# Performance work log

Measured on AMD Instinct MI355X. Metric: run time of the kernel, lower is better.

## Reference

```python
import jax, jax.numpy as jnp
import numpy as np

B, L = 4, 2048
D_MODEL, D_INNER, D_STATE, DT_RANK, D_CONV = 1024, 2048, 16, 64, 4


def setup_inputs() -> dict:
    key = jax.random.key(0)
    ks = jax.random.split(key, 10)
    s = lambda k, shape, sc: jax.random.normal(k, shape, dtype=jnp.float32) * sc
    return {
        "x": s(ks[0], (B, L, D_MODEL), 1.0),
        "W_in": s(ks[1], (2 * D_INNER, D_MODEL), D_MODEL ** -0.5),
        "conv_w": s(ks[2], (D_INNER, D_CONV), D_CONV ** -0.5),
        "conv_b": s(ks[3], (D_INNER,), 0.02),
        "A_log": jnp.log(jnp.arange(1, D_STATE + 1, dtype=jnp.float32)),
        "D": jnp.ones((D_INNER,), dtype=jnp.float32),
        "W_x": s(ks[4], (DT_RANK + 2 * D_STATE, D_INNER), D_INNER ** -0.5),
        "W_dt": s(ks[5], (D_INNER, DT_RANK), DT_RANK ** -0.5),
        "b_dt": s(ks[6], (D_INNER,), 0.02) - 4.0,  # softplus -> small positive dt
        "W_out": s(ks[7], (D_MODEL, D_INNER), D_INNER ** -0.5),
    }


def reference(x, W_in, conv_w, conv_b, A_log, D, W_x, W_dt, b_dt, W_out):
    Bb, Ll, _ = x.shape
    # input projection, split into ssm branch and gate branch
    xz = x @ W_in.T                       # (B, L, 2*Di)
    xr, z = jnp.split(xz, 2, axis=-1)     # (B, L, Di) each
    # depthwise causal conv1d (torch pads both sides then slices [:L])
    xc = jax.lax.conv_general_dilated(
        xr.transpose(0, 2, 1),            # (B, Di, L)
        conv_w[:, None, :],               # (Di, 1, K)
        window_strides=(1,),
        padding=[(D_CONV - 1, 0)],
        dimension_numbers=("NCH", "OIH", "NCH"),
        feature_group_count=D_INNER,
    ) + conv_b[None, :, None]
    xs = jax.nn.silu(xc.transpose(0, 2, 1))  # (B, L, Di)
    # input-dependent dt, B, C
    x_dbl = xs @ W_x.T                        # (B, L, dt_rank + 2*S)
    dt_r, b_sel, c_sel = jnp.split(x_dbl, [DT_RANK, DT_RANK + D_STATE], axis=-1)
    dt = jax.nn.softplus(dt_r @ W_dt.T + b_dt)  # (B, L, Di)
    a_diag = -jnp.exp(A_log)                    # (S,)

    def step(h, inp):
        dt_t, b_t, c_t, x_t = inp                       # (B,Di),(B,S),(B,S),(B,Di)
        a_bar = jnp.exp(dt_t[:, :, None] * a_diag)      # (B, Di, S)
        h = a_bar * h + (dt_t * x_t)[:, :, None] * b_t[:, None, :]
        y = jnp.einsum("bds,bs->bd", h, c_t) + D * x_t
        return h, y

    h0 = jnp.zeros((Bb, D_INNER, D_STATE), dtype=x.dtype)
    _, ys = jax.lax.scan(
        step, h0,
        (dt.transpose(1, 0, 2), b_sel.transpose(1, 0, 2),
         c_sel.transpose(1, 0, 2), xs.transpose(1, 0, 2)),
    )
    y = ys.transpose(1, 0, 2)                           # (B, L, Di)
    return (y * jax.nn.silu(z)) @ W_out.T               # (B, L, d_model)
```

## Files before the change

kernel.cpp:

```cpp
#include <hip/hip_runtime.h>
#include <math.h>

typedef unsigned short u16;
typedef unsigned int u32;

constexpr int Bb = 4, Ll = 2048, DM = 1024, DI = 2048, DS = 16, DTR = 64, KC = 4;
constexpr int M = Bb * Ll;
constexpr int NPAD = 128;
constexpr int NCHUNK = 16;
constexpr int LC = Ll / NCHUNK;
constexpr int LDXZ = 4096;

__device__ __forceinline__ float b2f(u16 u) {
    return __uint_as_float(((u32)u) << 16);
}
__device__ __forceinline__ u16 f2b(float f) {
    u32 x = __float_as_uint(f);
    u32 r = (x + 0x7fffu + ((x >> 16) & 1u)) >> 16;
    return (u16)r;
}

typedef __attribute__((ext_vector_type(8))) short short8;
typedef __attribute__((ext_vector_type(4))) short short4v;
typedef __attribute__((ext_vector_type(4))) float floatx4;

__device__ __forceinline__ void gload16(const u16* g, u16* l) {
    __builtin_amdgcn_global_load_lds(
        (const __attribute__((address_space(1))) void*)g,
        (__attribute__((address_space(3))) void*)l,
        16, 0, 0);
}

__device__ __forceinline__ void pow_tree(float a, float* aa) {
    float a2 = a * a, a4 = a2 * a2, a8 = a4 * a4;
    aa[0] = a;        aa[1] = a2;       aa[2] = a * a2;   aa[3] = a4;
    aa[4] = a * a4;   aa[5] = a2 * a4;  aa[6] = aa[2] * a4; aa[7] = a8;
    aa[8] = a * a8;   aa[9] = a2 * a8;  aa[10] = aa[2] * a8; aa[11] = a4 * a8;
    aa[12] = aa[4] * a8; aa[13] = aa[5] * a8; aa[14] = aa[6] * a8; aa[15] = a8 * a8;
}

template<int OUTM>
__global__ __launch_bounds__(512, 2) void gemm256(
    const u16* __restrict__ A, const u16* __restrict__ Bm,
    void* __restrict__ Cv,
    int K, int lda, int ldb, int ldc)
{
    __shared__ alignas(16) u16 ldsA[4][256 * 32];
    __shared__ alignas(16) u16 ldsB[4][256 * 32];

    const int lane = threadIdx.x & 63;
    const int wave = threadIdx.x >> 6;
    const int wr = wave >> 2;
    const int wc = wave & 3;
    const int m0 = blockIdx.y * 256;
    const int n0 = blockIdx.x * 256;

    const int lrow = lane >> 2;
    const int skc  = (((lane & 3) + (lane >> 3)) & 3) * 8;
    const u16* pA = A  + (size_t)(m0 + wave * 32 + lrow) * lda + skc;
    const u16* pB = Bm + (size_t)(n0 + wave * 32 + lrow) * ldb + skc;
    const int ldst = wave * 1024;

    const int r16 = lane & 15;
    const int quad = lane >> 4;
    const int slot = (quad + 4 - ((r16 >> 1) & 3)) & 3;
    const int aoff = (wr * 128 + r16) * 32 + slot * 8;
    const int boff = (wc * 64  + r16) * 32 + slot * 8;

    const int NT = K >> 5;

    floatx4 acc[8][4] = {};

#pragma unroll
    for (int t = 0; t < 3; ++t) {
        gload16(pA + t * 32,            &ldsA[t][ldst]);
        gload16(pA + t * 32 + 16 * lda, &ldsA[t][ldst + 512]);
        gload16(pB + t * 32,            &ldsB[t][ldst]);
        gload16(pB + t * 32 + 16 * ldb, &ldsB[t][ldst + 512]);
    }
    asm volatile("s_waitcnt vmcnt(8)" ::: "memory");
    __builtin_amdgcn_sched_barrier(0);
    __builtin_amdgcn_s_barrier();

    for (int t = 0; t < NT; ++t) {
        const u16* la = &ldsA[t & 3][aoff];
        const u16* lb = &ldsB[t & 3][boff];
        short8 af[8], bf[4];

#pragma unroll
        for (int i = 0; i < 4; ++i) af[i] = *(const short8*)(la + i * 512);
#pragma unroll
        for (int j = 0; j < 4; ++j) bf[j] = *(const short8*)(lb + j * 512);
        if (t + 3 < NT) {
            const u16* s = pA + (t + 3) * 32;
            u16* d = &ldsA[(t + 3) & 3][ldst];
            gload16(s, d);
            gload16(s + 16 * lda, d + 512);
        }
        __builtin_amdgcn_sched_barrier(0);
        __builtin_amdgcn_s_barrier();
        asm volatile("s_waitcnt lgkmcnt(0)" ::: "memory");
        __builtin_amdgcn_sched_barrier(0);
        __builtin_amdgcn_s_setprio(1);
#pragma unroll
        for (int i = 0; i < 4; ++i)
#pragma unroll
            for (int j = 0; j < 4; ++j)
                acc[i][j] = __builtin_amdgcn_mfma_f32_16x16x32_bf16(
                    af[i], bf[j], acc[i][j], 0, 0, 0);
        __builtin_amdgcn_s_setprio(0);
        __builtin_amdgcn_sched_barrier(0);
        __builtin_amdgcn_s_barrier();

#pragma unroll
        for (int i = 4; i < 8; ++i) af[i] = *(const short8*)(la + i * 512);
        if (t + 3 < NT) {
            const u16* s = pB + (t + 3) * 32;
            u16* d = &ldsB[(t + 3) & 3][ldst];
            gload16(s, d);
            gload16(s + 16 * ldb, d + 512);
        }
        __builtin_amdgcn_sched_barrier(0);
        __builtin_amdgcn_s_barrier();
        asm volatile("s_waitcnt lgkmcnt(0)" ::: "memory");
        __builtin_amdgcn_sched_barrier(0);
        __builtin_amdgcn_s_setprio(1);
#pragma unroll
        for (int i = 4; i < 8; ++i)
#pragma unroll
            for (int j = 0; j < 4; ++j)
                acc[i][j] = __builtin_amdgcn_mfma_f32_16x16x32_bf16(
                    af[i], bf[j], acc[i][j], 0, 0, 0);
        __builtin_amdgcn_s_setprio(0);
        if (t + 3 < NT)      asm volatile("s_waitcnt vmcnt(8)" ::: "memory");
        else if (t + 2 < NT) asm volatile("s_waitcnt vmcnt(4)" ::: "memory");
        else if (t + 1 < NT) asm volatile("s_waitcnt vmcnt(0)" ::: "memory");
        __builtin_amdgcn_sched_barrier(0);
        __builtin_amdgcn_s_barrier();
    }

    const int mw = m0 + wr * 128;
    const int nw = n0 + wc * 64;
    const int rb = quad * 4;
#pragma unroll
    for (int i = 0; i < 8; ++i) {
#pragma unroll
        for (int j = 0; j < 4; ++j) {
            const int n = nw + j * 16 + r16;
#pragma unroll
            for (int r = 0; r < 4; ++r) {
                const int m = mw + i * 16 + rb + r;
                float v = acc[i][j][r];
                if (OUTM == 1)
                    ((float*)Cv)[(size_t)m * ldc + n] = v;
                else
                    ((u16*)Cv)[(size_t)m * ldc + n] = f2b(v);
            }
        }
    }
}

template<int OUTM>
__global__ __launch_bounds__(512, 2) void gemm256n128(
    const u16* __restrict__ A, const u16* __restrict__ Bm,
    void* __restrict__ Cv,
    int K, int lda, int ldb, int ldc)
{
    __shared__ alignas(16) u16 ldsA[4][256 * 32];
    __shared__ alignas(16) u16 ldsB[4][128 * 32];

    const int lane = threadIdx.x & 63;
    const int wave = threadIdx.x >> 6;
    const int wr = wave >> 1;
    const int wc = wave & 1;
    const int m0 = blockIdx.y * 256;
    const int n0 = blockIdx.x * 128;

    const int lrow = lane >> 2;
    const int skc  = (((lane & 3) + (lane >> 3)) & 3) * 8;
    const u16* pA = A  + (size_t)(m0 + wave * 32 + lrow) * lda + skc;
    const u16* pB = Bm + (size_t)(n0 + wave * 16 + lrow) * ldb + skc;
    const int ldstA = wave * 1024;
    const int ldstB = wave * 512;

    const int r16 = lane & 15;
    const int quad = lane >> 4;
    const int slot = (quad + 4 - ((r16 >> 1) & 3)) & 3;
    const int aoff = (wr * 64 + r16) * 32 + slot * 8;
    const int boff = (wc * 64 + r16) * 32 + slot * 8;

    const int NT = K >> 5;

    floatx4 acc[4][4] = {};

#pragma unroll
    for (int t = 0; t < 3; ++t) {
        gload16(pA + t * 32,            &ldsA[t][ldstA]);
        gload16(pA + t * 32 + 16 * lda, &ldsA[t][ldstA + 512]);
        gload16(pB + t * 32,            &ldsB[t][ldstB]);
    }
    asm volatile("s_waitcnt vmcnt(6)" ::: "memory");
    __builtin_amdgcn_sched_barrier(0);
    __builtin_amdgcn_s_barrier();

    for (int t = 0; t < NT; ++t) {
        const u16* la = &ldsA[t & 3][aoff];
        const u16* lb = &ldsB[t & 3][boff];
        short8 af[4], bf[4];
#pragma unroll
        for (int i = 0; i < 4; ++i) af[i] = *(const short8*)(la + i * 512);
#pragma unroll
        for (int j = 0; j < 4; ++j) bf[j] = *(const short8*)(lb + j * 512);
        if (t + 3 < NT) {
            const u16* sa = pA + (t + 3) * 32;
            u16* da = &ldsA[(t + 3) & 3][ldstA];
            gload16(sa, da);
            gload16(sa + 16 * lda, da + 512);
            gload16(pB + (t + 3) * 32, &ldsB[(t + 3) & 3][ldstB]);
        }
        __builtin_amdgcn_sched_barrier(0);
        __builtin_amdgcn_s_barrier();
        asm volatile("s_waitcnt lgkmcnt(0)" ::: "memory");
        __builtin_amdgcn_sched_barrier(0);
        __builtin_amdgcn_s_setprio(1);
#pragma unroll
        for (int i = 0; i < 4; ++i)
#pragma unroll
            for (int j = 0; j < 4; ++j)
                acc[i][j] = __builtin_amdgcn_mfma_f32_16x16x32_bf16(
                    af[i], bf[j], acc[i][j], 0, 0, 0);
        __builtin_amdgcn_s_setprio(0);
        if (t + 3 < NT)      asm volatile("s_waitcnt vmcnt(6)" ::: "memory");
        else if (t + 2 < NT) asm volatile("s_waitcnt vmcnt(3)" ::: "memory");
        else if (t + 1 < NT) asm volatile("s_waitcnt vmcnt(0)" ::: "memory");
        __builtin_amdgcn_sched_barrier(0);
        __builtin_amdgcn_s_barrier();
    }

    const int mw = m0 + wr * 64;
    const int nw = n0 + wc * 64;
    const int rb = quad * 4;
#pragma unroll
    for (int i = 0; i < 4; ++i) {
#pragma unroll
        for (int j = 0; j < 4; ++j) {
            const int n = nw + j * 16 + r16;
#pragma unroll
            for (int r = 0; r < 4; ++r) {
                const int m = mw + i * 16 + rb + r;
                float v = acc[i][j][r];
                if (OUTM == 1)
                    ((float*)Cv)[(size_t)m * ldc + n] = v;
                else
                    ((u16*)Cv)[(size_t)m * ldc + n] = f2b(v);
            }
        }
    }
}

template<int OUTM>
__global__ __launch_bounds__(256) void gemm_bt(
    const u16* __restrict__ A, const u16* __restrict__ Bm,
    void* __restrict__ Cv, const float* __restrict__ bias,
    int K, int lda, int ldb, int ldc)
{
    __shared__ alignas(16) u16 ldsA[128 * 32];
    __shared__ alignas(16) u16 ldsB[128 * 32];

    const int lane = threadIdx.x & 63;
    const int wave = threadIdx.x >> 6;
    const int wr = wave >> 1, wc = wave & 1;
    const int m0 = blockIdx.y * 128;
    const int n0 = blockIdx.x * 128;
    const int koff = (OUTM == 4) ? blockIdx.z * K : 0;

    const int srow = wave * 32 + (lane >> 2);
    const int skc  = (((lane & 3) + (lane >> 3)) & 3) * 8;
    const u16* Ag = A + (size_t)(m0 + srow) * lda + skc + koff;
    const u16* Bg = Bm + (size_t)(n0 + srow) * ldb + skc + koff;
    u16* lA = &ldsA[wave * 1024];
    u16* lB = &ldsB[wave * 1024];

    const int r16 = lane & 15;
    const int quad = lane >> 4;
    const int slot = (quad + 4 - ((r16 >> 1) & 3)) & 3;
    const u16* arow = &ldsA[(wr * 64 + r16) * 32 + slot * 8];
    const u16* brow = &ldsB[(wc * 64 + r16) * 32 + slot * 8];

    floatx4 acc[4][4] = {};

    for (int k0 = 0; k0 < K; k0 += 32) {
        gload16(Ag + k0,                    lA);
        gload16(Ag + k0 + (size_t)16 * lda, lA + 512);
        gload16(Bg + k0,                    lB);
        gload16(Bg + k0 + (size_t)16 * ldb, lB + 512);
        __syncthreads();

        short8 af[4], bf[4];
#pragma unroll
        for (int i = 0; i < 4; i++) af[i] = *(const short8*)(arow + i * 16 * 32);
#pragma unroll
        for (int j = 0; j < 4; j++) bf[j] = *(const short8*)(brow + j * 16 * 32);
#pragma unroll
        for (int i = 0; i < 4; i++)
#pragma unroll
            for (int j = 0; j < 4; j++)
                acc[i][j] = __builtin_amdgcn_mfma_f32_16x16x32_bf16(
                    af[i], bf[j], acc[i][j], 0, 0, 0);
        __syncthreads();
    }

    const int mw = m0 + wr * 64;
    const int nw = n0 + wc * 64;
    const int rb = quad * 4;
#pragma unroll
    for (int i = 0; i < 4; i++) {
#pragma unroll
        for (int j = 0; j < 4; j++) {
            const int n = nw + j * 16 + r16;
#pragma unroll
            for (int r = 0; r < 4; r++) {
                const int m = mw + i * 16 + rb + r;
                float v = acc[i][j][r];
                if (OUTM == 2) {
                    v += bias[n];
                    v = (v > 20.f) ? v : log1pf(__expf(v));
                }
                if (OUTM == 4)
                    ((float*)Cv)[((size_t)blockIdx.z * M + m) * ldc + n] = v;
                else if (OUTM == 1)
                    ((float*)Cv)[(size_t)m * ldc + n] = v;
                else
                    ((u16*)Cv)[(size_t)m * ldc + n] = f2b(v);
            }
        }
    }
}

__global__ __launch_bounds__(256) void redk_gemm3(
    const float* __restrict__ part, u16* __restrict__ xdbl,
    float* __restrict__ bcf)
{
    const int t = blockIdx.x * 256 + threadIdx.x;
    const int n4 = (t & 31) * 4;
    const int m = t >> 5;
    const size_t stride = (size_t)M * NPAD;
    const float* p = part + (size_t)m * NPAD + n4;
    floatx4 acc = *(const floatx4*)(p)
                + *(const floatx4*)(p + stride)
                + *(const floatx4*)(p + 2 * stride)
                + *(const floatx4*)(p + 3 * stride);
    short4v ob;
#pragma unroll
    for (int j = 0; j < 4; j++) ob[j] = (short)f2b(acc[j]);
    *(short4v*)(xdbl + (size_t)m * NPAD + n4) = ob;
    if (n4 >= 64 && n4 < 96)
        *(floatx4*)(bcf + (size_t)m * 32 + (n4 - 64)) = acc;
}

__global__ __launch_bounds__(256) void cvt_f2b(
    const float* __restrict__ in, u16* __restrict__ out, int n)
{
    int i = blockIdx.x * blockDim.x + threadIdx.x;
    if (i < n) out[i] = f2b(in[i]);
}

__global__ __launch_bounds__(256) void prep_weights(
    const float* __restrict__ W_in, const float* __restrict__ W_x,
    const float* __restrict__ W_dt, const float* __restrict__ W_out,
    u16* __restrict__ wibf, u16* __restrict__ wxp,
    u16* __restrict__ wdtb, u16* __restrict__ woutb)
{
    constexpr int N1 = 2 * DI * DM;
    constexpr int N2 = NPAD * DI;
    constexpr int N3 = DI * DTR;
    int idx = blockIdx.x * blockDim.x + threadIdx.x;
    if (idx < N1) {
        wibf[idx] = f2b(W_in[idx]);
    } else if (idx < N1 + N2) {
        int i = idx - N1;
        int r = i >> 11, c = i & 2047;
        wxp[i] = (r < 96) ? f2b(W_x[r * 2048 + c]) : (u16)0;
    } else if (idx < N1 + N2 + N3) {
        int i = idx - N1 - N2;
        wdtb[i] = f2b(W_dt[i]);
    } else {
        int i = idx - N1 - N2 - N3;
        woutb[i] = f2b(W_out[i]);
    }
}

__global__ __launch_bounds__(256) void conv_silu(
    const u16* __restrict__ xz, const float* __restrict__ conv_w,
    const float* __restrict__ conv_b, u16* __restrict__ xs)
{
    const int m = blockIdx.x;
    const int d0 = threadIdx.x * 8;
    const int l = m & (Ll - 1);

    float acc[8];
    {
        floatx4 cb0 = *(const floatx4*)(conv_b + d0);
        floatx4 cb1 = *(const floatx4*)(conv_b + d0 + 4);
#pragma unroll
        for (int j = 0; j < 4; j++) { acc[j] = cb0[j]; acc[4 + j] = cb1[j]; }
    }
    float w[8][KC];
#pragma unroll
    for (int jd = 0; jd < 8; jd++) {
        floatx4 wv = *(const floatx4*)(conv_w + (d0 + jd) * KC);
#pragma unroll
        for (int k = 0; k < KC; k++) w[jd][k] = wv[k];
    }
#pragma unroll
    for (int k = 0; k < KC; k++) {
        int li = l - (KC - 1) + k;
        if (li >= 0) {
            short8 xv = *(const short8*)(xz + (size_t)(m - (KC - 1) + k) * LDXZ + d0);
#pragma unroll
            for (int jd = 0; jd < 8; jd++)
                acc[jd] += b2f((u16)xv[jd]) * w[jd][k];
        }
    }
    short8 o;
#pragma unroll
    for (int jd = 0; jd < 8; jd++) {
        float s = acc[jd] / (1.f + __expf(-acc[jd]));
        o[jd] = (short)f2b(s);
    }
    *(short8*)(xs + (size_t)m * DI + d0) = o;
}

__global__ __launch_bounds__(256) void scan_p1(
    const u16* __restrict__ xzdt, const u16* __restrict__ xs,
    const float* __restrict__ bcf, const float* __restrict__ A_log,
    float* __restrict__ scr_P, float* __restrict__ scr_hend)
{
    __shared__ alignas(16) float bcs[LC * 32];

    const int d = blockIdx.x * 256 + threadIdx.x;
    const int b = blockIdx.y;
    const int c = blockIdx.z;
    const int m0 = b * Ll + c * LC;

    {
        const float* bc_g = bcf + (size_t)m0 * 32;
#pragma unroll
        for (int j = 0; j < 4; j++) {
            int idx = j * 1024 + threadIdx.x * 4;
            *(floatx4*)(bcs + idx) = *(const floatx4*)(bc_g + idx);
        }
    }

    const float ad0 = -__expf(A_log[0]);
    float adl[DS];
    bool fast = true;
#pragma unroll
    for (int s = 0; s < DS; s++) {
        float av = -__expf(A_log[s]);
        adl[s] = av;
        float kr = (float)(s + 1);
        if (fabsf(av / ad0 - kr) > 1e-4f * kr) fast = false;
    }

    const u16* dt_p = xzdt + (size_t)m0 * LDXZ + d;
    const u16* xs_p = xs + (size_t)m0 * DI + d;

    float h[DS] = {};
    float P[DS];
#pragma unroll
    for (int s = 0; s < DS; s++) P[s] = 1.f;
    float sdt = 0.f;

    __syncthreads();

    u16 dt_c = dt_p[0],     xs_c = xs_p[0];
    u16 dt_1 = dt_p[LDXZ],  xs_1 = xs_p[DI];

    if (fast) {
        for (int l = 0; l < LC; l++) {
            u16 dt_2 = dt_p[2 * LDXZ];
            u16 xs_2 = xs_p[2 * DI];
            const float* bl = bcs + l * 32;
            floatx4 B0 = *(const floatx4*)(bl);
            floatx4 B1 = *(const floatx4*)(bl + 4);
            floatx4 B2 = *(const floatx4*)(bl + 8);
            floatx4 B3 = *(const floatx4*)(bl + 12);

            float dtv = b2f(dt_c);
            float xv  = b2f(xs_c);
            float bx = dtv * xv;
            sdt += dtv;
            float aa[DS];
            pow_tree(__expf(dtv * ad0), aa);
#pragma unroll
            for (int s = 0; s < DS; s++) {
                float Bv = (s < 4) ? B0[s] : (s < 8) ? B1[s - 4]
                         : (s < 12) ? B2[s - 8] : B3[s - 12];
                h[s] = aa[s] * h[s] + bx * Bv;
            }
            dt_c = dt_1; dt_1 = dt_2; xs_c = xs_1; xs_1 = xs_2;
            dt_p += LDXZ; xs_p += DI;
        }
        pow_tree(__expf(ad0 * sdt), P);
    } else {
        for (int l = 0; l < LC; l++) {
            u16 dt_2 = dt_p[2 * LDXZ];
            u16 xs_2 = xs_p[2 * DI];
            const float* bl = bcs + l * 32;
            floatx4 B0 = *(const floatx4*)(bl);
            floatx4 B1 = *(const floatx4*)(bl + 4);
            floatx4 B2 = *(const floatx4*)(bl + 8);
            floatx4 B3 = *(const floatx4*)(bl + 12);

            float dtv = b2f(dt_c);
            float xv  = b2f(xs_c);
            float bx = dtv * xv;
#pragma unroll
            for (int s = 0; s < DS; s++) {
                float Bv = (s < 4) ? B0[s] : (s < 8) ? B1[s - 4]
                         : (s < 12) ? B2[s - 8] : B3[s - 12];
                float a = __expf(dtv * adl[s]);
                h[s] = a * h[s] + bx * Bv;
                P[s] *= a;
            }
            dt_c = dt_1; dt_1 = dt_2; xs_c = xs_1; xs_1 = xs_2;
            dt_p += LDXZ; xs_p += DI;
        }
    }

    const size_t base = ((size_t)(b * NCHUNK + c) * DI + d) * DS;
#pragma unroll
    for (int s = 0; s < DS; s += 4) {
        floatx4 pv = {P[s], P[s+1], P[s+2], P[s+3]};
        floatx4 hv = {h[s], h[s+1], h[s+2], h[s+3]};
        *(floatx4*)(scr_P + base + s)    = pv;
        *(floatx4*)(scr_hend + base + s) = hv;
    }
}

__global__ __launch_bounds__(256) void scan_p2(
    float* __restrict__ scr_P, const float* __restrict__ scr_hend)
{
    const int t = blockIdx.x * 256 + threadIdx.x;
    const int s = t & 15;
    const int d = (t >> 4) & (DI - 1);
    const int b = t >> 15;

    float hin = 0.f;
    for (int c = 0; c < NCHUNK; c++) {
        const size_t base = ((size_t)(b * NCHUNK + c) * DI + d) * DS + s;
        float p = scr_P[base];
        float he = scr_hend[base];
        scr_P[base] = hin;
        hin = p * hin + he;
    }
}

__global__ __launch_bounds__(256) void scan_p3(
    const u16* __restrict__ xz, const u16* xs, const float* __restrict__ bcf,
    const float* __restrict__ scr_hin, const float* __restrict__ A_log,
    const float* __restrict__ Dvec, u16* yg)
{
    __shared__ alignas(16) float bcs[LC * 32];

    const int d = blockIdx.x * 256 + threadIdx.x;
    const int b = blockIdx.y;
    const int c = blockIdx.z;
    const int m0 = b * Ll + c * LC;

    {
        const float* bc_g = bcf + (size_t)m0 * 32;
#pragma unroll
        for (int j = 0; j < 4; j++) {
            int idx = j * 1024 + threadIdx.x * 4;
            *(floatx4*)(bcs + idx) = *(const floatx4*)(bc_g + idx);
        }
    }

    const float ad0 = -__expf(A_log[0]);
    float adl[DS];
    bool fast = true;
#pragma unroll
    for (int s = 0; s < DS; s++) {
        float av = -__expf(A_log[s]);
        adl[s] = av;
        float kr = (float)(s + 1);
        if (fabsf(av / ad0 - kr) > 1e-4f * kr) fast = false;
    }
    const float Dd = Dvec[d];

    const u16* dt_p = xz + (size_t)m0 * LDXZ + d;
    const u16* z_p  = xz + (size_t)m0 * LDXZ + 2048 + d;
    const u16* xs_p = xs + (size_t)m0 * DI + d;
    u16* yg_p = yg + (size_t)m0 * DI + d;

    float h[DS];
    const size_t base = ((size_t)(b * NCHUNK + c) * DI + d) * DS;
#pragma unroll
    for (int s = 0; s < DS; s += 4) {
        floatx4 hv = *(const floatx4*)(scr_hin + base + s);
        h[s] = hv[0]; h[s+1] = hv[1]; h[s+2] = hv[2]; h[s+3] = hv[3];
    }

    __syncthreads();

    u16 dt_c = dt_p[0],    dt_1 = dt_p[LDXZ];
    u16 xs_c = xs_p[0],    xs_1 = xs_p[DI];
    u16 z_c  = z_p[0],     z_1  = z_p[LDXZ];

    for (int l = 0; l < LC; l++) {
        u16 dt_2 = dt_p[2 * LDXZ];
        u16 xs_2 = xs_p[2 * DI];
        u16 z_2  = z_p[2 * LDXZ];
        const float* bl = bcs + l * 32;
        floatx4 Bq[4], Cq[4];
#pragma unroll
        for (int q = 0; q < 4; q++) {
            Bq[q] = *(const floatx4*)(bl + q * 4);
            Cq[q] = *(const floatx4*)(bl + 16 + q * 4);
        }

        float dtv = b2f(dt_c);
        float xv  = b2f(xs_c);
        float bx = dtv * xv;
        float aa[DS];
        if (fast) {
            pow_tree(__expf(dtv * ad0), aa);
        } else {
#pragma unroll
            for (int s = 0; s < DS; s++) aa[s] = __expf(dtv * adl[s]);
        }
        float y0 = 0.f, y1 = 0.f, y2 = 0.f, y3 = 0.f;
#pragma unroll
        for (int q = 0; q < 4; q++) {
#pragma unroll
            for (int j = 0; j < 4; j++) {
                int s = q * 4 + j;
                h[s] = aa[s] * h[s] + bx * Bq[q][j];
            }
        }
#pragma unroll
        for (int j = 0; j < 4; j++) {
            y0 += h[j] * Cq[0][j];
            y1 += h[4 + j] * Cq[1][j];
            y2 += h[8 + j] * Cq[2][j];
            y3 += h[12 + j] * Cq[3][j];
        }
        float yt = ((y0 + y1) + (y2 + y3)) + Dd * xv;
        float zv = b2f(z_c);
        float g = zv / (1.f + __expf(-zv));
        yg_p[0] = f2b(yt * g);

        dt_c = dt_1; dt_1 = dt_2;
        xs_c = xs_1; xs_1 = xs_2;
        z_c  = z_1;  z_1  = z_2;
        dt_p += LDXZ; xs_p += DI; z_p += LDXZ; yg_p += DI;
    }
}

extern "C" void kernel_launch(void* const* d_in, const int* in_sizes, int n_in,
                              void* d_out, int out_size, void* d_ws, size_t ws_size,
                              hipStream_t stream)
{
    const float* x      = (const float*)d_in[0];
    const float* W_in   = (const float*)d_in[1];
    const float* conv_w = (const float*)d_in[2];
    const float* conv_b = (const float*)d_in[3];
    const float* A_log  = (const float*)d_in[4];
    const float* Dvec   = (const float*)d_in[5];
    const float* W_x    = (const float*)d_in[6];
    const float* W_dt   = (const float*)d_in[7];
    const float* b_dt   = (const float*)d_in[8];
    const float* W_out  = (const float*)d_in[9];

    u16* ws = (u16*)d_ws;
    u16* xz    = ws;                 ws += (size_t)M * LDXZ;
    u16* xs    = ws;                 ws += (size_t)M * DI;
    u16* xbf   = ws;                 ws += (size_t)M * DM;
    u16* wibf  = ws;                 ws += (size_t)2 * DI * DM;
    u16* wxp   = ws;                 ws += (size_t)NPAD * DI;
    u16* wdtb  = ws;                 ws += (size_t)DI * DTR;
    u16* woutb = ws;                 ws += (size_t)DM * DI;
    u16* xdbl  = ws;                 ws += (size_t)M * NPAD;
    u16* yg    = xs;
    float* part     = (float*)xbf;
    float* scr_P    = (float*)xbf;
    float* scr_hend = scr_P + (size_t)Bb * NCHUNK * DI * DS;
    float* bcf      = (float*)wibf;

    cvt_f2b<<<(M * DM) / 256, 256, 0, stream>>>(x, xbf, M * DM);
    {
        constexpr int NTOT = 2 * DI * DM + NPAD * DI + DI * DTR + DM * DI;
        prep_weights<<<NTOT / 256, 256, 0, stream>>>(
            W_in, W_x, W_dt, W_out, wibf, wxp, wdtb, woutb);
    }

    gemm256<0><<<dim3(LDXZ / 256, M / 256), 512, 0, stream>>>(
        xbf, wibf, xz, DM, DM, DM, LDXZ);

    conv_silu<<<M, 256, 0, stream>>>(xz, conv_w, conv_b, xs);

    gemm_bt<4><<<dim3(1, M / 128, 4), 256, 0, stream>>>(
        xs, wxp, part, nullptr, DI / 4, DI, DI, NPAD);
    redk_gemm3<<<(M * 32) / 256, 256, 0, stream>>>(part, xdbl, bcf);

    gemm_bt<2><<<dim3(DI / 128, M / 128), 256, 0, stream>>>(
        xdbl, wdtb, xz, b_dt, DTR, NPAD, DTR, LDXZ);

    scan_p1<<<dim3(DI / 256, Bb, NCHUNK), 256, 0, stream>>>(
        xz, xs, bcf, A_log, scr_P, scr_hend);
    scan_p2<<<(Bb * DI * DS) / 256, 256, 0, stream>>>(scr_P, scr_hend);
    scan_p3<<<dim3(DI / 256, Bb, NCHUNK), 256, 0, stream>>>(
        xz, xs, bcf, scr_P, A_log, Dvec, yg);

    gemm256n128<1><<<dim3(DM / 128, M / 256), 512, 0, stream>>>(
        yg, woutb, d_out, DI, DI, DI, DM);
}
```

Measured before the change: 479.8 us.

## Double scan chunks, store chunk dt sums, shrink out-proj LDS ring, fuse prep kernels

Doubles the number of scan chunks so the chunked scan passes expose more parallelism with shorter sequential loops. Chunk phase 1 now stores only end states plus per-chunk dt sums; phase 2 rebuilds the decay products as exp(A*sum dt) instead of loading a separate P array, which cuts scratch traffic. The output GEMM drops from a 4-stage to a 3-stage LDS ring to allow more resident blocks per CU, at the cost of a shallower prefetch. The input and weight bf16 conversion kernels are merged into one launch.

```diff
diff --git a/kernel.cpp b/kernel.cpp
--- a/kernel.cpp
+++ b/kernel.cpp
@@ -7,7 +7,7 @@
 constexpr int Bb = 4, Ll = 2048, DM = 1024, DI = 2048, DS = 16, DTR = 64, KC = 4;
 constexpr int M = Bb * Ll;
 constexpr int NPAD = 128;
-constexpr int NCHUNK = 16;
+constexpr int NCHUNK = 32;
 constexpr int LC = Ll / NCHUNK;
 constexpr int LDXZ = 4096;
 
@@ -161,13 +161,13 @@
 }
 
 template<int OUTM>
-__global__ __launch_bounds__(512, 2) void gemm256n128(
+__global__ __launch_bounds__(512, 4) void gemm256n128(
     const u16* __restrict__ A, const u16* __restrict__ Bm,
     void* __restrict__ Cv,
     int K, int lda, int ldb, int ldc)
 {
-    __shared__ alignas(16) u16 ldsA[4][256 * 32];
-    __shared__ alignas(16) u16 ldsB[4][128 * 32];
+    __shared__ alignas(16) u16 ldsA[3][256 * 32];
+    __shared__ alignas(16) u16 ldsB[3][128 * 32];
 
     const int lane = threadIdx.x & 63;
     const int wave = threadIdx.x >> 6;
@@ -194,29 +194,30 @@
     floatx4 acc[4][4] = {};
 
 #pragma unroll
-    for (int t = 0; t < 3; ++t) {
+    for (int t = 0; t < 2; ++t) {
         gload16(pA + t * 32,            &ldsA[t][ldstA]);
         gload16(pA + t * 32 + 16 * lda, &ldsA[t][ldstA + 512]);
         gload16(pB + t * 32,            &ldsB[t][ldstB]);
     }
-    asm volatile("s_waitcnt vmcnt(6)" ::: "memory");
+    asm volatile("s_waitcnt vmcnt(3)" ::: "memory");
     __builtin_amdgcn_sched_barrier(0);
     __builtin_amdgcn_s_barrier();
 
+    int bc = 0, bs = 2;
     for (int t = 0; t < NT; ++t) {
-        const u16* la = &ldsA[t & 3][aoff];
-        const u16* lb = &ldsB[t & 3][boff];
+        const u16* la = &ldsA[bc][aoff];
+        const u16* lb = &ldsB[bc][boff];
         short8 af[4], bf[4];
 #pragma unroll
         for (int i = 0; i < 4; ++i) af[i] = *(const short8*)(la + i * 512);
 #pragma unroll
         for (int j = 0; j < 4; ++j) bf[j] = *(const short8*)(lb + j * 512);
-        if (t + 3 < NT) {
-            const u16* sa = pA + (t + 3) * 32;
-            u16* da = &ldsA[(t + 3) & 3][ldstA];
+        if (t + 2 < NT) {
+            const u16* sa = pA + (t + 2) * 32;
+            u16* da = &ldsA[bs][ldstA];
             gload16(sa, da);
             gload16(sa + 16 * lda, da + 512);
-            gload16(pB + (t + 3) * 32, &ldsB[(t + 3) & 3][ldstB]);
+            gload16(pB + (t + 2) * 32, &ldsB[bs][ldstB]);
         }
         __builtin_amdgcn_sched_barrier(0);
         __builtin_amdgcn_s_barrier();
@@ -230,11 +231,12 @@
                 acc[i][j] = __builtin_amdgcn_mfma_f32_16x16x32_bf16(
                     af[i], bf[j], acc[i][j], 0, 0, 0);
         __builtin_amdgcn_s_setprio(0);
-        if (t + 3 < NT)      asm volatile("s_waitcnt vmcnt(6)" ::: "memory");
-        else if (t + 2 < NT) asm volatile("s_waitcnt vmcnt(3)" ::: "memory");
+        if (t + 2 < NT)      asm volatile("s_waitcnt vmcnt(3)" ::: "memory");
         else if (t + 1 < NT) asm volatile("s_waitcnt vmcnt(0)" ::: "memory");
         __builtin_amdgcn_sched_barrier(0);
         __builtin_amdgcn_s_barrier();
+        bc = (bc == 2) ? 0 : bc + 1;
+        bs = (bs == 2) ? 0 : bs + 1;
     }
 
     const int mw = m0 + wr * 64;
@@ -358,23 +360,23 @@
         *(floatx4*)(bcf + (size_t)m * 32 + (n4 - 64)) = acc;
 }
 
-__global__ __launch_bounds__(256) void cvt_f2b(
-    const float* __restrict__ in, u16* __restrict__ out, int n)
-{
-    int i = blockIdx.x * blockDim.x + threadIdx.x;
-    if (i < n) out[i] = f2b(in[i]);
-}
-
-__global__ __launch_bounds__(256) void prep_weights(
-    const float* __restrict__ W_in, const float* __restrict__ W_x,
-    const float* __restrict__ W_dt, const float* __restrict__ W_out,
-    u16* __restrict__ wibf, u16* __restrict__ wxp,
+__global__ __launch_bounds__(256) void prep_all(
+    const float* __restrict__ x, const float* __restrict__ W_in,
+    const float* __restrict__ W_x, const float* __restrict__ W_dt,
+    const float* __restrict__ W_out,
+    u16* __restrict__ xbf, u16* __restrict__ wibf, u16* __restrict__ wxp,
     u16* __restrict__ wdtb, u16* __restrict__ woutb)
 {
+    constexpr int N0 = M * DM;
     constexpr int N1 = 2 * DI * DM;
     constexpr int N2 = NPAD * DI;
     constexpr int N3 = DI * DTR;
     int idx = blockIdx.x * blockDim.x + threadIdx.x;
+    if (idx < N0) {
+        xbf[idx] = f2b(x[idx]);
+        return;
+    }
+    idx -= N0;
     if (idx < N1) {
         wibf[idx] = f2b(W_in[idx]);
     } else if (idx < N1 + N2) {
@@ -434,7 +436,7 @@
 __global__ __launch_bounds__(256) void scan_p1(
     const u16* __restrict__ xzdt, const u16* __restrict__ xs,
     const float* __restrict__ bcf, const float* __restrict__ A_log,
-    float* __restrict__ scr_P, float* __restrict__ scr_hend)
+    float* __restrict__ scr_h, float* __restrict__ sdt_g)
 {
     __shared__ alignas(16) float bcs[LC * 32];
 
@@ -446,7 +448,7 @@
     {
         const float* bc_g = bcf + (size_t)m0 * 32;
 #pragma unroll
-        for (int j = 0; j < 4; j++) {
+        for (int j = 0; j < 2; j++) {
             int idx = j * 1024 + threadIdx.x * 4;
             *(floatx4*)(bcs + idx) = *(const floatx4*)(bc_g + idx);
         }
@@ -467,9 +469,6 @@
     const u16* xs_p = xs + (size_t)m0 * DI + d;
 
     float h[DS] = {};
-    float P[DS];
-#pragma unroll
-    for (int s = 0; s < DS; s++) P[s] = 1.f;
     float sdt = 0.f;
 
     __syncthreads();
@@ -502,7 +501,6 @@
             dt_c = dt_1; dt_1 = dt_2; xs_c = xs_1; xs_1 = xs_2;
             dt_p += LDXZ; xs_p += DI;
         }
-        pow_tree(__expf(ad0 * sdt), P);
     } else {
         for (int l = 0; l < LC; l++) {
             u16 dt_2 = dt_p[2 * LDXZ];
@@ -516,13 +514,13 @@
             float dtv = b2f(dt_c);
             float xv  = b2f(xs_c);
             float bx = dtv * xv;
+            sdt += dtv;
 #pragma unroll
             for (int s = 0; s < DS; s++) {
                 float Bv = (s < 4) ? B0[s] : (s < 8) ? B1[s - 4]
                          : (s < 12) ? B2[s - 8] : B3[s - 12];
                 float a = __expf(dtv * adl[s]);
                 h[s] = a * h[s] + bx * Bv;
-                P[s] *= a;
             }
             dt_c = dt_1; dt_1 = dt_2; xs_c = xs_1; xs_1 = xs_2;
             dt_p += LDXZ; xs_p += DI;
@@ -532,28 +530,37 @@
     const size_t base = ((size_t)(b * NCHUNK + c) * DI + d) * DS;
 #pragma unroll
     for (int s = 0; s < DS; s += 4) {
-        floatx4 pv = {P[s], P[s+1], P[s+2], P[s+3]};
         floatx4 hv = {h[s], h[s+1], h[s+2], h[s+3]};
-        *(floatx4*)(scr_P + base + s)    = pv;
-        *(floatx4*)(scr_hend + base + s) = hv;
-    }
+        *(floatx4*)(scr_h + base + s) = hv;
+    }
+    sdt_g[(size_t)(b * NCHUNK + c) * DI + d] = sdt;
 }
 
 __global__ __launch_bounds__(256) void scan_p2(
-    float* __restrict__ scr_P, const float* __restrict__ scr_hend)
+    float* __restrict__ scr_h, const float* __restrict__ sdt_g,
+    const float* __restrict__ A_log)
 {
     const int t = blockIdx.x * 256 + threadIdx.x;
     const int s = t & 15;
     const int d = (t >> 4) & (DI - 1);
     const int b = t >> 15;
-
-    float hin = 0.f;
+    const float adl = -__expf(A_log[s]);
+
+    float he[NCHUNK], P[NCHUNK];
+#pragma unroll
     for (int c = 0; c < NCHUNK; c++) {
         const size_t base = ((size_t)(b * NCHUNK + c) * DI + d) * DS + s;
-        float p = scr_P[base];
-        float he = scr_hend[base];
-        scr_P[base] = hin;
-        hin = p * hin + he;
+        he[c] = scr_h[base];
+        P[c] = adl * sdt_g[(size_t)(b * NCHUNK + c) * DI + d];
+    }
+#pragma unroll
+    for (int c = 0; c < NCHUNK; c++) P[c] = __expf(P[c]);
+    float hin = 0.f;
+#pragma unroll
+    for (int c = 0; c < NCHUNK; c++) {
+        const size_t base = ((size_t)(b * NCHUNK + c) * DI + d) * DS + s;
+        scr_h[base] = hin;
+        hin = P[c] * hin + he[c];
     }
 }
 
@@ -572,7 +579,7 @@
     {
         const float* bc_g = bcf + (size_t)m0 * 32;
 #pragma unroll
-        for (int j = 0; j < 4; j++) {
+        for (int j = 0; j < 2; j++) {
             int idx = j * 1024 + threadIdx.x * 4;
             *(floatx4*)(bcs + idx) = *(const floatx4*)(bc_g + idx);
         }
@@ -684,16 +691,15 @@
     u16* woutb = ws;                 ws += (size_t)DM * DI;
     u16* xdbl  = ws;                 ws += (size_t)M * NPAD;
     u16* yg    = xs;
-    float* part     = (float*)xbf;
-    float* scr_P    = (float*)xbf;
-    float* scr_hend = scr_P + (size_t)Bb * NCHUNK * DI * DS;
-    float* bcf      = (float*)wibf;
-
-    cvt_f2b<<<(M * DM) / 256, 256, 0, stream>>>(x, xbf, M * DM);
+    float* part  = (float*)xbf;
+    float* scr_h = (float*)xbf;
+    float* bcf   = (float*)wibf;
+    float* sdt_g = bcf + (size_t)M * 32;
+
     {
-        constexpr int NTOT = 2 * DI * DM + NPAD * DI + DI * DTR + DM * DI;
-        prep_weights<<<NTOT / 256, 256, 0, stream>>>(
-            W_in, W_x, W_dt, W_out, wibf, wxp, wdtb, woutb);
+        constexpr int NTOT = M * DM + 2 * DI * DM + NPAD * DI + DI * DTR + DM * DI;
+        prep_all<<<NTOT / 256, 256, 0, stream>>>(
+            x, W_in, W_x, W_dt, W_out, xbf, wibf, wxp, wdtb, woutb);
     }
 
     gemm256<0><<<dim3(LDXZ / 256, M / 256), 512, 0, stream>>>(
@@ -709,10 +715,10 @@
         xdbl, wdtb, xz, b_dt, DTR, NPAD, DTR, LDXZ);
 
     scan_p1<<<dim3(DI / 256, Bb, NCHUNK), 256, 0, stream>>>(
-        xz, xs, bcf, A_log, scr_P, scr_hend);
-    scan_p2<<<(Bb * DI * DS) / 256, 256, 0, stream>>>(scr_P, scr_hend);
+        xz, xs, bcf, A_log, scr_h, sdt_g);
+    scan_p2<<<(Bb * DI * DS) / 256, 256, 0, stream>>>(scr_h, sdt_g, A_log);
     scan_p3<<<dim3(DI / 256, Bb, NCHUNK), 256, 0, stream>>>(
-        xz, xs, bcf, scr_P, A_log, Dvec, yg);
+        xz, xs, bcf, scr_h, A_log, Dvec, yg);
 
     gemm256n128<1><<<dim3(DM / 128, M / 256), 512, 0, stream>>>(
         yg, woutb, d_out, DI, DI, DI, DM);
```

Result: no change. 476.1 us (-0.8%).
